# Performance work log

Measured on AMD Instinct MI355X. Metric: run time of the kernel, lower is better.

## Reference

```python
import jax, jax.numpy as jnp
import numpy as np

B, N_IN, N_OUT = 8192, 2048, 2048


def setup_inputs() -> dict:
    key = jax.random.key(0)
    kx, kw = jax.random.split(key)
    x = jax.random.normal(kx, (B, N_IN), dtype=jnp.float32)
    # torch: uniform_(-0.5, 0.5)
    weight = jax.random.uniform(kw, (N_IN, N_OUT), dtype=jnp.float32, minval=-0.5, maxval=0.5)
    return {"x": x, "weight": weight}


def reference(x, weight):
    # Binarize: W > 0 -> {0, 1}; then dense matmul (batch, n_in) @ (n_in, n_out)
    w_bin = (weight > 0).astype(x.dtype)
    return x @ w_bin
```

## Files before the change

kernel.cpp:

```cpp
#include <hip/hip_runtime.h>


#define MDIM 8192
#define NDIM 2048
#define KDIM 2048
#define NT   (KDIM / 128)

typedef __attribute__((ext_vector_type(8))) short short8;
typedef __attribute__((ext_vector_type(4))) float float4v;
typedef __attribute__((ext_vector_type(4))) float f32x4;
typedef __attribute__((ext_vector_type(4))) int int4v;
typedef __attribute__((ext_vector_type(4))) unsigned short ushort4v;
typedef __attribute__((ext_vector_type(8))) unsigned short ushort8v;

__device__ __forceinline__ unsigned short f2bf(float f) {
    union { float f; unsigned u; } v; v.f = f;
    unsigned r = v.u + 0x7FFFu + ((v.u >> 16) & 1u);
    return (unsigned short)(r >> 16);
}

__device__ __forceinline__ void gload_lds16(void* l, const void* g) {
    __builtin_amdgcn_global_load_lds(
        (const __attribute__((address_space(1))) unsigned int*)g,
        (__attribute__((address_space(3))) unsigned int*)l,
        16, 0, 0);
}

#define FENCE asm volatile("" ::: "memory")
#define BAR do { FENCE; __builtin_amdgcn_s_barrier(); FENCE; } while (0)

__global__ __launch_bounds__(256) void prep(const float* __restrict__ X,
                                            const float* __restrict__ W,
                                            signed char* __restrict__ Xq,
                                            signed char* __restrict__ Wt,
                                            float* __restrict__ Sc) {
    __shared__ __align__(16) signed char T[64][80];
    __shared__ float wm[4];
    const int t = threadIdx.x;
    const int bid = blockIdx.x;

    if (bid < MDIM) {
        const int row = bid;
        const float* xr = X + (size_t)row * KDIM + t * 8;
        float4v a = *reinterpret_cast<const float4v*>(xr);
        float4v b = *reinterpret_cast<const float4v*>(xr + 4);
        float m = fabsf(a[0]);
        m = fmaxf(m, fabsf(a[1])); m = fmaxf(m, fabsf(a[2])); m = fmaxf(m, fabsf(a[3]));
        m = fmaxf(m, fabsf(b[0])); m = fmaxf(m, fabsf(b[1]));
        m = fmaxf(m, fabsf(b[2])); m = fmaxf(m, fabsf(b[3]));
#pragma unroll
        for (int off = 32; off; off >>= 1)
            m = fmaxf(m, __shfl_xor(m, off));
        if ((t & 63) == 0) wm[t >> 6] = m;
        __syncthreads();
        const float s = fmaxf(fmaxf(wm[0], wm[1]), fmaxf(wm[2], wm[3]));
        const float inv = (s > 0.f) ? 127.0f / s : 0.f;

        int q[8];
        q[0] = __float2int_rn(a[0] * inv); q[1] = __float2int_rn(a[1] * inv);
        q[2] = __float2int_rn(a[2] * inv); q[3] = __float2int_rn(a[3] * inv);
        q[4] = __float2int_rn(b[0] * inv); q[5] = __float2int_rn(b[1] * inv);
        q[6] = __float2int_rn(b[2] * inv); q[7] = __float2int_rn(b[3] * inv);
        unsigned lo = (q[0] & 255) | ((q[1] & 255) << 8) | ((q[2] & 255) << 16) | ((unsigned)(q[3] & 255) << 24);
        unsigned hi = (q[4] & 255) | ((q[5] & 255) << 8) | ((q[6] & 255) << 16) | ((unsigned)(q[7] & 255) << 24);
        unsigned* dst = (unsigned*)(Xq + (size_t)row * KDIM + t * 8);
        dst[0] = lo; dst[1] = hi;
        if (t == 0) Sc[row] = s * (1.0f / 127.0f);
    } else {
        const int wb = bid - MDIM;
        const int k0 = (wb >> 5) * 64;
        const int n0 = (wb & 31) * 64;
        const int kr = t >> 4;
        const int nc = (t & 15) * 4;
#pragma unroll
        for (int rr = 0; rr < 4; ++rr) {
            int k = k0 + rr * 16 + kr;
            float4v w4 = *reinterpret_cast<const float4v*>(W + (size_t)k * NDIM + n0 + nc);
#pragma unroll
            for (int c = 0; c < 4; ++c)
                T[nc + c][rr * 16 + kr] = (w4[c] > 0.0f) ? (signed char)1 : (signed char)0;
        }
        __syncthreads();
        const int row = t >> 2, ch = t & 3;
        int4v v = *reinterpret_cast<const int4v*>(&T[row][ch * 16]);
        *reinterpret_cast<int4v*>(Wt + (size_t)(n0 + row) * KDIM + k0 + ch * 16) = v;
    }
}

__global__ __launch_bounds__(1024, 4) void gemm_mb(const signed char* __restrict__ A,
                                                   const signed char* __restrict__ Bt,
                                                   const float* __restrict__ Sc,
                                                   float* __restrict__ O) {
    extern __shared__ char lds[];
    const int tid  = threadIdx.x;
    const int lane = tid & 63;
    const int w    = tid >> 6;
    const int wr   = w >> 2;
    const int wc   = w & 3;

    int id  = blockIdx.x;
    int swz = (id & 7) * 32 + (id >> 3);
    const int bm = swz >> 3;
    const int bn = swz & 7;

    const int l3 = lane >> 3, l7 = lane & 7;
    const int srcOff = (w * 16 + l3) * KDIM + ((l7 ^ l3) << 4);
    const char* gA = (const char*)A + (size_t)(bm * 256) * KDIM + srcOff;
    const char* gB = (const char*)Bt + (size_t)(bn * 256) * KDIM + srcOff;

    const int fr = lane & 15, fg = lane >> 4;
    const int se0 = ((fg)     ^ (fr & 7)) << 4;
    const int se1 = ((4 + fg) ^ (fr & 7)) << 4;
    const int aRd = (wr * 64 + fr) * 128;
    const int bRd = 32768 + (wc * 64 + fr) * 128;

    int4v acc[4][4];
#pragma unroll
    for (int i = 0; i < 4; ++i)
#pragma unroll
        for (int j = 0; j < 4; ++j) {
            acc[i][j][0] = 0; acc[i][j][1] = 0; acc[i][j][2] = 0; acc[i][j][3] = 0;
        }

    gload_lds16(lds + w * 2048,              gA);
    gload_lds16(lds + w * 2048 + 1024,       gA + (size_t)8 * KDIM);
    gload_lds16(lds + 32768 + w * 2048,      gB);
    gload_lds16(lds + 32768 + w * 2048 + 1024, gB + (size_t)8 * KDIM);

    for (int t = 0; t < NT; ++t) {
        const int cur = (t & 1) << 16;
        const int nxt = ((t + 1) & 1) << 16;
        const bool more = (t + 1 < NT);
        const char* gAs = gA + (size_t)(t + 1) * 128;
        const char* gBs = gB + (size_t)(t + 1) * 128;

        asm volatile("s_waitcnt vmcnt(0)" ::: "memory");
        BAR;

        if (more) {
            gload_lds16(lds + nxt + w * 2048,                gAs);
            gload_lds16(lds + nxt + w * 2048 + 1024,         gAs + (size_t)8 * KDIM);
            gload_lds16(lds + nxt + 32768 + w * 2048,        gBs);
            gload_lds16(lds + nxt + 32768 + w * 2048 + 1024, gBs + (size_t)8 * KDIM);
        }

        int4v af[4], bf[4];
#pragma unroll
        for (int mi = 0; mi < 4; ++mi)
            af[mi] = *reinterpret_cast<const int4v*>(lds + cur + aRd + mi * 2048 + se0);
#pragma unroll
        for (int ni = 0; ni < 4; ++ni)
            bf[ni] = *reinterpret_cast<const int4v*>(lds + cur + bRd + ni * 2048 + se0);
        __builtin_amdgcn_s_setprio(1);
#pragma unroll
        for (int mi = 0; mi < 4; ++mi)
#pragma unroll
            for (int ni = 0; ni < 4; ++ni)
                acc[mi][ni] = __builtin_amdgcn_mfma_i32_16x16x64_i8(
                    af[mi], bf[ni], acc[mi][ni], 0, 0, 0);
        __builtin_amdgcn_s_setprio(0);

#pragma unroll
        for (int mi = 0; mi < 4; ++mi)
            af[mi] = *reinterpret_cast<const int4v*>(lds + cur + aRd + mi * 2048 + se1);
#pragma unroll
        for (int ni = 0; ni < 4; ++ni)
            bf[ni] = *reinterpret_cast<const int4v*>(lds + cur + bRd + ni * 2048 + se1);
        __builtin_amdgcn_s_setprio(1);
#pragma unroll
        for (int mi = 0; mi < 4; ++mi)
#pragma unroll
            for (int ni = 0; ni < 4; ++ni)
                acc[mi][ni] = __builtin_amdgcn_mfma_i32_16x16x64_i8(
                    af[mi], bf[ni], acc[mi][ni], 0, 0, 0);
        __builtin_amdgcn_s_setprio(0);
        FENCE;
    }

    const int orow0 = bm * 256 + wr * 64 + fg * 4;
    const int ocol0 = bn * 256 + wc * 64 + fr;
#pragma unroll
    for (int mi = 0; mi < 4; ++mi)
#pragma unroll
        for (int r = 0; r < 4; ++r) {
            const int row = orow0 + mi * 16 + r;
            const float s = Sc[row];
            float* op = O + (size_t)row * NDIM + ocol0;
#pragma unroll
            for (int ni = 0; ni < 4; ++ni)
                op[ni * 16] = s * (float)acc[mi][ni][r];
        }
}

__global__ __launch_bounds__(256, 2) void binlin_fused(
        const float* __restrict__ X, const float* __restrict__ W,
        float* __restrict__ O) {
    const int tid = threadIdx.x;
    const int lane = tid & 63;
    const int wave = tid >> 6;
    const int wr = wave >> 1, wc = wave & 1;
    const int NWG = (MDIM / 128) * (NDIM / 128);
    int id = blockIdx.x;
    int swz = (id & 7) * (NWG >> 3) + (id >> 3);
    const int bm = swz >> 4, bn = swz & 15;

    __shared__ __align__(16) unsigned short As[128][40];
    __shared__ __align__(16) unsigned short Bs[128][40];

    const int rA = tid >> 3, kA = (tid & 7) * 4;
    const float* aPtr = X + (size_t)(bm * 128 + rA) * KDIM + kA;
    const int nB = (tid & 31) * 4, kB = (tid >> 5) * 4;
    const float* bPtr = W + (size_t)kB * NDIM + (size_t)bn * 128 + nB;

    float4v aReg[4], bReg[4];
#pragma unroll
    for (int p = 0; p < 4; ++p)
        aReg[p] = *reinterpret_cast<const float4v*>(aPtr + (size_t)(32 * p) * KDIM);
#pragma unroll
    for (int dk = 0; dk < 4; ++dk)
        bReg[dk] = *reinterpret_cast<const float4v*>(bPtr + (size_t)dk * NDIM);

    f32x4 acc[4][4];
#pragma unroll
    for (int i = 0; i < 4; ++i)
#pragma unroll
        for (int j = 0; j < 4; ++j) {
            acc[i][j][0] = 0.f; acc[i][j][1] = 0.f; acc[i][j][2] = 0.f; acc[i][j][3] = 0.f;
        }

    const int r16 = lane & 15, g8 = (lane >> 4) * 8;
    for (int kt = 0; kt < KDIM; kt += 32) {
#pragma unroll
        for (int p = 0; p < 4; ++p) {
            ushort4v v;
            v[0] = f2bf(aReg[p][0]); v[1] = f2bf(aReg[p][1]);
            v[2] = f2bf(aReg[p][2]); v[3] = f2bf(aReg[p][3]);
            *reinterpret_cast<ushort4v*>(&As[rA + 32 * p][kA]) = v;
        }
        unsigned short bb[4][4];
#pragma unroll
        for (int dk = 0; dk < 4; ++dk)
#pragma unroll
            for (int dn = 0; dn < 4; ++dn)
                bb[dn][dk] = (bReg[dk][dn] > 0.0f) ? (unsigned short)0x3F80u
                                                   : (unsigned short)0u;
#pragma unroll
        for (int dn = 0; dn < 4; ++dn) {
            ushort4v v;
            v[0] = bb[dn][0]; v[1] = bb[dn][1]; v[2] = bb[dn][2]; v[3] = bb[dn][3];
            *reinterpret_cast<ushort4v*>(&Bs[nB + dn][kB]) = v;
        }
        __syncthreads();
        if (kt + 32 < KDIM) {
#pragma unroll
            for (int p = 0; p < 4; ++p)
                aReg[p] = *reinterpret_cast<const float4v*>(
                    aPtr + (size_t)(32 * p) * KDIM + (kt + 32));
#pragma unroll
            for (int dk = 0; dk < 4; ++dk)
                bReg[dk] = *reinterpret_cast<const float4v*>(
                    bPtr + (size_t)(kt + 32 + dk) * NDIM);
        }
        short8 af[4], bfv[4];
#pragma unroll
        for (int mi = 0; mi < 4; ++mi)
            af[mi] = *reinterpret_cast<const short8*>(&As[wr * 64 + mi * 16 + r16][g8]);
#pragma unroll
        for (int ni = 0; ni < 4; ++ni)
            bfv[ni] = *reinterpret_cast<const short8*>(&Bs[wc * 64 + ni * 16 + r16][g8]);
#pragma unroll
        for (int mi = 0; mi < 4; ++mi)
#pragma unroll
            for (int ni = 0; ni < 4; ++ni)
                acc[mi][ni] = __builtin_amdgcn_mfma_f32_16x16x32_bf16(
                    af[mi], bfv[ni], acc[mi][ni], 0, 0, 0);
        __syncthreads();
    }

    const int orow0 = bm * 128 + wr * 64 + (lane >> 4) * 4;
    const int ocol0 = bn * 128 + wc * 64 + r16;
#pragma unroll
    for (int mi = 0; mi < 4; ++mi)
#pragma unroll
        for (int ni = 0; ni < 4; ++ni)
#pragma unroll
            for (int r = 0; r < 4; ++r)
                O[(size_t)(orow0 + mi * 16 + r) * NDIM + ocol0 + ni * 16] =
                    acc[mi][ni][r];
}

extern "C" void kernel_launch(void* const* d_in, const int* in_sizes, int n_in,
                              void* d_out, int out_size, void* d_ws, size_t ws_size,
                              hipStream_t stream) {
    const float* X = (const float*)d_in[0];
    const float* W = (const float*)d_in[1];
    float* O = (float*)d_out;
    (void)in_sizes; (void)n_in; (void)out_size;

    const size_t xq_bytes = (size_t)MDIM * KDIM;
    const size_t wt_bytes = (size_t)NDIM * KDIM;
    const size_t sc_bytes = (size_t)MDIM * sizeof(float);
    const size_t need = xq_bytes + wt_bytes + sc_bytes;

    if (ws_size >= need) {
        signed char* Xq = (signed char*)d_ws;
        signed char* Wt = Xq + xq_bytes;
        float* Sc = (float*)(Wt + wt_bytes);
        hipFuncSetAttribute((const void*)gemm_mb,
                            hipFuncAttributeMaxDynamicSharedMemorySize, 131072);
        prep<<<dim3(MDIM + (KDIM / 64) * (NDIM / 64)), dim3(256), 0, stream>>>(X, W, Xq, Wt, Sc);
        gemm_mb<<<dim3((MDIM / 256) * (NDIM / 256)), dim3(1024), 131072, stream>>>(Xq, Wt, Sc, O);
    } else {
        binlin_fused<<<dim3((MDIM / 128) * (NDIM / 128)), dim3(256), 0, stream>>>(X, W, O);
    }
}
```

Before: 55.63 us.

## Split 256x256 GEMM block into two sequential 256x128 halves with 512 threads

The int8 GEMM kernel now uses 512 threads (8 waves), each workgroup computing its 256x256 output tile as two successive 256x128 halves that reuse the same A rows. LDS per buffer shrinks to 48KB, and the first K-slice of the second half is prefetched during the last iteration of the first half so the pipeline carries across. The aim is lower LDS use and fewer waves per block to reduce barrier cost. In exchange A is reloaded from global/L2 twice and per-wave MFMA parallelism per K-step is halved.

Result: slower. 59.21 us (+6.4%).

```diff
diff --git a/kernel.cpp b/kernel.cpp
--- a/kernel.cpp
+++ b/kernel.cpp
@@ -5,6 +5,8 @@
 #define NDIM 2048
 #define KDIM 2048
 #define NT   (KDIM / 128)
+#define CH   (64 * KDIM)
+#define BUFS 49152
 
 typedef __attribute__((ext_vector_type(8))) short short8;
 typedef __attribute__((ext_vector_type(4))) float float4v;
@@ -87,26 +89,25 @@
     }
 }
 
-__global__ __launch_bounds__(1024, 4) void gemm_mb(const signed char* __restrict__ A,
-                                                   const signed char* __restrict__ Bt,
-                                                   const float* __restrict__ Sc,
-                                                   float* __restrict__ O) {
+__global__ __launch_bounds__(512, 1) void gemm_2t(const signed char* __restrict__ A,
+                                                  const signed char* __restrict__ Bt,
+                                                  const float* __restrict__ Sc,
+                                                  float* __restrict__ O) {
     extern __shared__ char lds[];
     const int tid  = threadIdx.x;
     const int lane = tid & 63;
     const int w    = tid >> 6;
-    const int wr   = w >> 2;
-    const int wc   = w & 3;
+    const int wr   = w >> 1;
+    const int wc   = w & 1;
 
     int id  = blockIdx.x;
     int swz = (id & 7) * 32 + (id >> 3);
-    const int bm = swz >> 3;
-    const int bn = swz & 7;
+    const int bm  = swz >> 3;
+    const int bnh = swz & 7;
 
     const int l3 = lane >> 3, l7 = lane & 7;
-    const int srcOff = (w * 16 + l3) * KDIM + ((l7 ^ l3) << 4);
+    const int srcOff = (w * 8 + l3) * KDIM + ((l7 ^ l3) << 4);
     const char* gA = (const char*)A + (size_t)(bm * 256) * KDIM + srcOff;
-    const char* gB = (const char*)Bt + (size_t)(bn * 256) * KDIM + srcOff;
 
     const int fr = lane & 15, fg = lane >> 4;
     const int se0 = ((fg)     ^ (fr & 7)) << 4;
@@ -114,82 +115,102 @@
     const int aRd = (wr * 64 + fr) * 128;
     const int bRd = 32768 + (wc * 64 + fr) * 128;
 
-    int4v acc[4][4];
-#pragma unroll
-    for (int i = 0; i < 4; ++i)
-#pragma unroll
-        for (int j = 0; j < 4; ++j) {
-            acc[i][j][0] = 0; acc[i][j][1] = 0; acc[i][j][2] = 0; acc[i][j][3] = 0;
-        }
-
-    gload_lds16(lds + w * 2048,              gA);
-    gload_lds16(lds + w * 2048 + 1024,       gA + (size_t)8 * KDIM);
-    gload_lds16(lds + 32768 + w * 2048,      gB);
-    gload_lds16(lds + 32768 + w * 2048 + 1024, gB + (size_t)8 * KDIM);
-
-    for (int t = 0; t < NT; ++t) {
-        const int cur = (t & 1) << 16;
-        const int nxt = ((t + 1) & 1) << 16;
-        const bool more = (t + 1 < NT);
-        const char* gAs = gA + (size_t)(t + 1) * 128;
-        const char* gBs = gB + (size_t)(t + 1) * 128;
-
-        asm volatile("s_waitcnt vmcnt(0)" ::: "memory");
-        BAR;
-
-        if (more) {
-            gload_lds16(lds + nxt + w * 2048,                gAs);
-            gload_lds16(lds + nxt + w * 2048 + 1024,         gAs + (size_t)8 * KDIM);
-            gload_lds16(lds + nxt + 32768 + w * 2048,        gBs);
-            gload_lds16(lds + nxt + 32768 + w * 2048 + 1024, gBs + (size_t)8 * KDIM);
-        }
-
-        int4v af[4], bf[4];
+    {
+        const char* gB0 = (const char*)Bt + (size_t)(bnh * 256) * KDIM + srcOff;
+#pragma unroll
+        for (int c = 0; c < 4; ++c)
+            gload_lds16(lds + c * 8192 + w * 1024, gA + (size_t)c * CH);
+#pragma unroll
+        for (int c = 0; c < 2; ++c)
+            gload_lds16(lds + 32768 + c * 8192 + w * 1024, gB0 + (size_t)c * CH);
+    }
+
+    for (int tt = 0; tt < 2; ++tt) {
+        const char* gB  = (const char*)Bt + (size_t)(bnh * 256 + tt * 128) * KDIM + srcOff;
+        const char* gB2 = (const char*)Bt + (size_t)(bnh * 256 + 128) * KDIM + srcOff;
+
+        int4v acc[4][4];
+#pragma unroll
+        for (int i = 0; i < 4; ++i)
+#pragma unroll
+            for (int j = 0; j < 4; ++j) {
+                acc[i][j][0] = 0; acc[i][j][1] = 0; acc[i][j][2] = 0; acc[i][j][3] = 0;
+            }
+
+        for (int t = 0; t < NT; ++t) {
+            const int cur = (t & 1) * BUFS;
+            const int nxt = ((t + 1) & 1) * BUFS;
+
+            if (t == 0 && tt == 1) asm volatile("s_waitcnt vmcnt(63)" ::: "memory");
+            else                   asm volatile("s_waitcnt vmcnt(0)" ::: "memory");
+            BAR;
+
+            if (t + 1 < NT) {
+                const char* aN = gA + (size_t)(t + 1) * 128;
+                const char* bN = gB + (size_t)(t + 1) * 128;
+#pragma unroll
+                for (int c = 0; c < 4; ++c)
+                    gload_lds16(lds + nxt + c * 8192 + w * 1024, aN + (size_t)c * CH);
+#pragma unroll
+                for (int c = 0; c < 2; ++c)
+                    gload_lds16(lds + nxt + 32768 + c * 8192 + w * 1024, bN + (size_t)c * CH);
+            } else if (tt == 0) {
+#pragma unroll
+                for (int c = 0; c < 4; ++c)
+                    gload_lds16(lds + nxt + c * 8192 + w * 1024, gA + (size_t)c * CH);
+#pragma unroll
+                for (int c = 0; c < 2; ++c)
+                    gload_lds16(lds + nxt + 32768 + c * 8192 + w * 1024, gB2 + (size_t)c * CH);
+            }
+
+            int4v af[4], bf[4];
+#pragma unroll
+            for (int mi = 0; mi < 4; ++mi)
+                af[mi] = *reinterpret_cast<const int4v*>(lds + cur + aRd + mi * 2048 + se0);
+#pragma unroll
+            for (int ni = 0; ni < 4; ++ni)
+                bf[ni] = *reinterpret_cast<const int4v*>(lds + cur + bRd + ni * 2048 + se0);
+            __builtin_amdgcn_s_setprio(1);
+#pragma unroll
+            for (int mi = 0; mi < 4; ++mi)
+#pragma unroll
+                for (int ni = 0; ni < 4; ++ni)
+                    acc[mi][ni] = __builtin_amdgcn_mfma_i32_16x16x64_i8(
+                        af[mi], bf[ni], acc[mi][ni], 0, 0, 0);
+            __builtin_amdgcn_s_setprio(0);
+
+#pragma unroll
+            for (int mi = 0; mi < 4; ++mi)
+                af[mi] = *reinterpret_cast<const int4v*>(lds + cur + aRd + mi * 2048 + se1);
+#pragma unroll
+            for (int ni = 0; ni < 4; ++ni)
+                bf[ni] = *reinterpret_cast<const int4v*>(lds + cur + bRd + ni * 2048 + se1);
+            __builtin_amdgcn_s_setprio(1);
+#pragma unroll
+            for (int mi = 0; mi < 4; ++mi)
+#pragma unroll
+                for (int ni = 0; ni < 4; ++ni)
+                    acc[mi][ni] = __builtin_amdgcn_mfma_i32_16x16x64_i8(
+                        af[mi], bf[ni], acc[mi][ni], 0, 0, 0);
+            __builtin_amdgcn_s_setprio(0);
+            FENCE;
+        }
+
+        const int orow0 = bm * 256 + wr * 64 + fg * 4;
+        const int ocol0 = bnh * 256 + tt * 128 + wc * 64 + fr;
 #pragma unroll
         for (int mi = 0; mi < 4; ++mi)
-            af[mi] = *reinterpret_cast<const int4v*>(lds + cur + aRd + mi * 2048 + se0);
-#pragma unroll
-        for (int ni = 0; ni < 4; ++ni)
-            bf[ni] = *reinterpret_cast<const int4v*>(lds + cur + bRd + ni * 2048 + se0);
-        __builtin_amdgcn_s_setprio(1);
-#pragma unroll
-        for (int mi = 0; mi < 4; ++mi)
-#pragma unroll
-            for (int ni = 0; ni < 4; ++ni)
-                acc[mi][ni] = __builtin_amdgcn_mfma_i32_16x16x64_i8(
-                    af[mi], bf[ni], acc[mi][ni], 0, 0, 0);
-        __builtin_amdgcn_s_setprio(0);
-
-#pragma unroll
-        for (int mi = 0; mi < 4; ++mi)
-            af[mi] = *reinterpret_cast<const int4v*>(lds + cur + aRd + mi * 2048 + se1);
-#pragma unroll
-        for (int ni = 0; ni < 4; ++ni)
-            bf[ni] = *reinterpret_cast<const int4v*>(lds + cur + bRd + ni * 2048 + se1);
-        __builtin_amdgcn_s_setprio(1);
-#pragma unroll
-        for (int mi = 0; mi < 4; ++mi)
-#pragma unroll
-            for (int ni = 0; ni < 4; ++ni)
-                acc[mi][ni] = __builtin_amdgcn_mfma_i32_16x16x64_i8(
-                    af[mi], bf[ni], acc[mi][ni], 0, 0, 0);
-        __builtin_amdgcn_s_setprio(0);
+#pragma unroll
+            for (int r = 0; r < 4; ++r) {
+                const int row = orow0 + mi * 16 + r;
+                const float s = Sc[row];
+                float* op = O + (size_t)row * NDIM + ocol0;
+#pragma unroll
+                for (int ni = 0; ni < 4; ++ni)
+                    op[ni * 16] = s * (float)acc[mi][ni][r];
+            }
         FENCE;
     }
-
-    const int orow0 = bm * 256 + wr * 64 + fg * 4;
-    const int ocol0 = bn * 256 + wc * 64 + fr;
-#pragma unroll
-    for (int mi = 0; mi < 4; ++mi)
-#pragma unroll
-        for (int r = 0; r < 4; ++r) {
-            const int row = orow0 + mi * 16 + r;
-            const float s = Sc[row];
-            float* op = O + (size_t)row * NDIM + ocol0;
-#pragma unroll
-            for (int ni = 0; ni < 4; ++ni)
-                op[ni * 16] = s * (float)acc[mi][ni][r];
-        }
 }
 
 __global__ __launch_bounds__(256, 2) void binlin_fused(
@@ -306,10 +327,10 @@
         signed char* Xq = (signed char*)d_ws;
         signed char* Wt = Xq + xq_bytes;
         float* Sc = (float*)(Wt + wt_bytes);
-        hipFuncSetAttribute((const void*)gemm_mb,
-                            hipFuncAttributeMaxDynamicSharedMemorySize, 131072);
+        hipFuncSetAttribute((const void*)gemm_2t,
+                            hipFuncAttributeMaxDynamicSharedMemorySize, 98304);
         prep<<<dim3(MDIM + (KDIM / 64) * (NDIM / 64)), dim3(256), 0, stream>>>(X, W, Xq, Wt, Sc);
-        gemm_mb<<<dim3((MDIM / 256) * (NDIM / 256)), dim3(1024), 131072, stream>>>(Xq, Wt, Sc, O);
+        gemm_2t<<<dim3((MDIM / 256) * (NDIM / 256)), dim3(512), 98304, stream>>>(Xq, Wt, Sc, O);
     } else {
         binlin_fused<<<dim3((MDIM / 128) * (NDIM / 128)), dim3(256), 0, stream>>>(X, W, O);
     }
```

## Use 4 waves with 128x128 per-wave tiles in int8 GEMM

Applied to the files above, without the earlier changes.

Restructures the int8 MFMA GEMM from 16 waves per block, each computing a 64x64 sub-tile, to 4 waves per block, each computing a 128x128 sub-tile with 8x8 accumulators. Each wave now issues eight global-to-LDS loads per operand per stage instead of two. The aim is more register-level reuse of A/B fragments and fewer LDS reads per MFMA. The cost is 256 accumulator registers per wave, which may limit occupancy or cause spills, and fewer waves to hide latency.

New measurement: 59.94 us. 7.8% more time.

```diff
diff --git a/kernel.cpp b/kernel.cpp
--- a/kernel.cpp
+++ b/kernel.cpp
@@ -87,7 +87,7 @@
     }
 }
 
-__global__ __launch_bounds__(1024, 4) void gemm_mb(const signed char* __restrict__ A,
+__global__ __launch_bounds__(256, 1) void gemm_big(const signed char* __restrict__ A,
                                                    const signed char* __restrict__ Bt,
                                                    const float* __restrict__ Sc,
                                                    float* __restrict__ O) {
@@ -95,8 +95,8 @@
     const int tid  = threadIdx.x;
     const int lane = tid & 63;
     const int w    = tid >> 6;
-    const int wr   = w >> 2;
-    const int wc   = w & 3;
+    const int wr   = w >> 1;
+    const int wc   = w & 1;
 
     int id  = blockIdx.x;
     int swz = (id & 7) * 32 + (id >> 3);
@@ -104,90 +104,101 @@
     const int bn = swz & 7;
 
     const int l3 = lane >> 3, l7 = lane & 7;
-    const int srcOff = (w * 16 + l3) * KDIM + ((l7 ^ l3) << 4);
+    const int srcOff = (w * 64 + l3) * KDIM + ((l7 ^ l3) << 4);
     const char* gA = (const char*)A + (size_t)(bm * 256) * KDIM + srcOff;
     const char* gB = (const char*)Bt + (size_t)(bn * 256) * KDIM + srcOff;
+    const int ldsA = (w * 64) * 128;
+    const int ldsB = 32768 + (w * 64) * 128;
 
     const int fr = lane & 15, fg = lane >> 4;
     const int se0 = ((fg)     ^ (fr & 7)) << 4;
     const int se1 = ((4 + fg) ^ (fr & 7)) << 4;
-    const int aRd = (wr * 64 + fr) * 128;
-    const int bRd = 32768 + (wc * 64 + fr) * 128;
-
-    int4v acc[4][4];
-#pragma unroll
-    for (int i = 0; i < 4; ++i)
-#pragma unroll
-        for (int j = 0; j < 4; ++j) {
+    const int aRd = (wr * 128 + fr) * 128;
+    const int bRd = 32768 + (wc * 128 + fr) * 128;
+
+    int4v acc[8][8];
+#pragma unroll
+    for (int i = 0; i < 8; ++i)
+#pragma unroll
+        for (int j = 0; j < 8; ++j) {
             acc[i][j][0] = 0; acc[i][j][1] = 0; acc[i][j][2] = 0; acc[i][j][3] = 0;
         }
 
-    gload_lds16(lds + w * 2048,              gA);
-    gload_lds16(lds + w * 2048 + 1024,       gA + (size_t)8 * KDIM);
-    gload_lds16(lds + 32768 + w * 2048,      gB);
-    gload_lds16(lds + 32768 + w * 2048 + 1024, gB + (size_t)8 * KDIM);
+#pragma unroll
+    for (int i = 0; i < 8; ++i)
+        gload_lds16(lds + ldsA + i * 1024, gA + (size_t)i * 8 * KDIM);
+#pragma unroll
+    for (int i = 0; i < 8; ++i)
+        gload_lds16(lds + ldsB + i * 1024, gB + (size_t)i * 8 * KDIM);
 
     for (int t = 0; t < NT; ++t) {
         const int cur = (t & 1) << 16;
         const int nxt = ((t + 1) & 1) << 16;
         const bool more = (t + 1 < NT);
-        const char* gAs = gA + (size_t)(t + 1) * 128;
-        const char* gBs = gB + (size_t)(t + 1) * 128;
+        const char* aN = gA + (size_t)(t + 1) * 128;
+        const char* bN = gB + (size_t)(t + 1) * 128;
 
         asm volatile("s_waitcnt vmcnt(0)" ::: "memory");
         BAR;
 
         if (more) {
-            gload_lds16(lds + nxt + w * 2048,                gAs);
-            gload_lds16(lds + nxt + w * 2048 + 1024,         gAs + (size_t)8 * KDIM);
-            gload_lds16(lds + nxt + 32768 + w * 2048,        gBs);
-            gload_lds16(lds + nxt + 32768 + w * 2048 + 1024, gBs + (size_t)8 * KDIM);
-        }
-
-        int4v af[4], bf[4];
-#pragma unroll
-        for (int mi = 0; mi < 4; ++mi)
-            af[mi] = *reinterpret_cast<const int4v*>(lds + cur + aRd + mi * 2048 + se0);
-#pragma unroll
-        for (int ni = 0; ni < 4; ++ni)
-            bf[ni] = *reinterpret_cast<const int4v*>(lds + cur + bRd + ni * 2048 + se0);
-        __builtin_amdgcn_s_setprio(1);
-#pragma unroll
-        for (int mi = 0; mi < 4; ++mi)
-#pragma unroll
-            for (int ni = 0; ni < 4; ++ni)
-                acc[mi][ni] = __builtin_amdgcn_mfma_i32_16x16x64_i8(
-                    af[mi], bf[ni], acc[mi][ni], 0, 0, 0);
-        __builtin_amdgcn_s_setprio(0);
-
-#pragma unroll
-        for (int mi = 0; mi < 4; ++mi)
-            af[mi] = *reinterpret_cast<const int4v*>(lds + cur + aRd + mi * 2048 + se1);
-#pragma unroll
-        for (int ni = 0; ni < 4; ++ni)
-            bf[ni] = *reinterpret_cast<const int4v*>(lds + cur + bRd + ni * 2048 + se1);
-        __builtin_amdgcn_s_setprio(1);
-#pragma unroll
-        for (int mi = 0; mi < 4; ++mi)
-#pragma unroll
-            for (int ni = 0; ni < 4; ++ni)
-                acc[mi][ni] = __builtin_amdgcn_mfma_i32_16x16x64_i8(
-                    af[mi], bf[ni], acc[mi][ni], 0, 0, 0);
-        __builtin_amdgcn_s_setprio(0);
+#pragma unroll
+            for (int i = 0; i < 8; ++i)
+                gload_lds16(lds + nxt + ldsA + i * 1024, aN + (size_t)i * 8 * KDIM);
+#pragma unroll
+            for (int i = 0; i < 8; ++i)
+                gload_lds16(lds + nxt + ldsB + i * 1024, bN + (size_t)i * 8 * KDIM);
+        }
+
+        {
+            int4v af[8], bf[8];
+#pragma unroll
+            for (int mi = 0; mi < 8; ++mi)
+                af[mi] = *reinterpret_cast<const int4v*>(lds + cur + aRd + mi * 2048 + se0);
+#pragma unroll
+            for (int ni = 0; ni < 8; ++ni)
+                bf[ni] = *reinterpret_cast<const int4v*>(lds + cur + bRd + ni * 2048 + se0);
+            __builtin_amdgcn_s_setprio(1);
+#pragma unroll
+            for (int mi = 0; mi < 8; ++mi)
+#pragma unroll
+                for (int ni = 0; ni < 8; ++ni)
+                    acc[mi][ni] = __builtin_amdgcn_mfma_i32_16x16x64_i8(
+                        af[mi], bf[ni], acc[mi][ni], 0, 0, 0);
+            __builtin_amdgcn_s_setprio(0);
+        }
+
+        {
+            int4v af[8], bf[8];
+#pragma unroll
+            for (int mi = 0; mi < 8; ++mi)
+                af[mi] = *reinterpret_cast<const int4v*>(lds + cur + aRd + mi * 2048 + se1);
+#pragma unroll
+            for (int ni = 0; ni < 8; ++ni)
+                bf[ni] = *reinterpret_cast<const int4v*>(lds + cur + bRd + ni * 2048 + se1);
+            __builtin_amdgcn_s_setprio(1);
+#pragma unroll
+            for (int mi = 0; mi < 8; ++mi)
+#pragma unroll
+                for (int ni = 0; ni < 8; ++ni)
+                    acc[mi][ni] = __builtin_amdgcn_mfma_i32_16x16x64_i8(
+                        af[mi], bf[ni], acc[mi][ni], 0, 0, 0);
+            __builtin_amdgcn_s_setprio(0);
+        }
         FENCE;
     }
 
-    const int orow0 = bm * 256 + wr * 64 + fg * 4;
-    const int ocol0 = bn * 256 + wc * 64 + fr;
-#pragma unroll
-    for (int mi = 0; mi < 4; ++mi)
+    const int orow0 = bm * 256 + wr * 128 + fg * 4;
+    const int ocol0 = bn * 256 + wc * 128 + fr;
+#pragma unroll
+    for (int mi = 0; mi < 8; ++mi)
 #pragma unroll
         for (int r = 0; r < 4; ++r) {
             const int row = orow0 + mi * 16 + r;
             const float s = Sc[row];
             float* op = O + (size_t)row * NDIM + ocol0;
 #pragma unroll
-            for (int ni = 0; ni < 4; ++ni)
+            for (int ni = 0; ni < 8; ++ni)
                 op[ni * 16] = s * (float)acc[mi][ni][r];
         }
 }
@@ -306,10 +317,10 @@
         signed char* Xq = (signed char*)d_ws;
         signed char* Wt = Xq + xq_bytes;
         float* Sc = (float*)(Wt + wt_bytes);
-        hipFuncSetAttribute((const void*)gemm_mb,
+        hipFuncSetAttribute((const void*)gemm_big,
                             hipFuncAttributeMaxDynamicSharedMemorySize, 131072);
         prep<<<dim3(MDIM + (KDIM / 64) * (NDIM / 64)), dim3(256), 0, stream>>>(X, W, Xq, Wt, Sc);
-        gemm_mb<<<dim3((MDIM / 256) * (NDIM / 256)), dim3(1024), 131072, stream>>>(Xq, Wt, Sc, O);
+        gemm_big<<<dim3((MDIM / 256) * (NDIM / 256)), dim3(256), 131072, stream>>>(Xq, Wt, Sc, O);
     } else {
         binlin_fused<<<dim3((MDIM / 128) * (NDIM / 128)), dim3(256), 0, stream>>>(X, W, O);
     }
```
